# Kernel tuning notes

Measured on AMD Instinct MI355X. Metric: run time of the kernel, lower is better.

Reference implementation:

```python
import jax, jax.numpy as jnp
import numpy as np

NUM_NODES = 2048
NUM_UNITS = 64
INPUT_DIM = 2
MAX_K = 2  # max_diffusion_step


def setup_inputs() -> dict:
    key = jax.random.key(0)
    ks = jax.random.split(key, 8)
    B, N, U, D = 32, NUM_NODES, NUM_UNITS, INPUT_DIM
    C = D + U                      # input_size after concat = 66
    M = 2 * MAX_K + 1              # num_matrices = 5
    w_scale = 1.0 / np.sqrt(C * M)
    return {
        "inputs": jax.random.normal(ks[0], (B, N * D), dtype=jnp.float32),
        "hx": jax.random.normal(ks[1], (B, N * U), dtype=jnp.float32),
        # row-stochastic-ish random-walk supports (scaled so K hops stay bounded)
        "support0": jax.random.uniform(ks[2], (N, N), dtype=jnp.float32) / N,
        "support1": jax.random.uniform(ks[3], (N, N), dtype=jnp.float32) / N,
        "W_ru": jax.random.normal(ks[4], (C * M, 2 * U), dtype=jnp.float32) * w_scale,
        "b_ru": jnp.full((2 * U,), 1.0, dtype=jnp.float32),   # bias_start=1.0
        "W_c": jax.random.normal(ks[5], (C * M, U), dtype=jnp.float32) * w_scale,
        "b_c": jnp.zeros((U,), dtype=jnp.float32),            # bias_start=0.0
    }


def _gconv(inputs, state, supports, W, b, output_size):
    # inputs: [B, N*D], state: [B, N*U]
    B = inputs.shape[0]
    N = NUM_NODES
    x0 = jnp.concatenate(
        [inputs.reshape(B, N, -1), state.reshape(B, N, -1)], axis=2
    )  # [B, N, C]
    C = x0.shape[2]
    xs = [x0]
    for S in supports:  # Chebyshev-style diffusion per support
        x1 = jnp.einsum("nm,bmc->bnc", S, x0)
        xs.append(x1)
        xk1, xk2 = x1, x0
        for _ in range(2, MAX_K + 1):
            x2 = 2.0 * jnp.einsum("nm,bmc->bnc", S, xk1) - xk2
            xs.append(x2)
            xk1, xk2 = x2, xk1
    M = len(xs)  # num_matrices
    # stack on new leading axis then permute(1,2,3,0): feature-major, matrix-minor
    x = jnp.stack(xs, axis=0).transpose(1, 2, 3, 0).reshape(B * N, C * M)
    out = x @ W + b  # [B*N, output_size]
    return out.reshape(B, N * output_size)


def reference(inputs, hx, support0, support1, W_ru, b_ru, W_c, b_c):
    B = inputs.shape[0]
    N, U = NUM_NODES, NUM_UNITS
    supports = (support0, support1)
    value = jax.nn.sigmoid(_gconv(inputs, hx, supports, W_ru, b_ru, 2 * U))
    value = value.reshape(B, N, 2 * U)
    r = value[..., :U].reshape(B, N * U)
    u = value[..., U:].reshape(B, N * U)
    c = jnp.tanh(_gconv(inputs, r * hx, supports, W_c, b_c, U))
    new_state = u * hx + (1.0 - u) * c
    return new_state
```

## Files before the change

kernel.cpp:

```cpp
#include <hip/hip_runtime.h>
#include <hip/hip_bf16.h>
#include <cstdint>
#include <cstddef>

typedef unsigned short u16;
typedef unsigned char u8;
using f32x4 = __attribute__((ext_vector_type(4))) float;
using s16x8 = __attribute__((ext_vector_type(8))) short;
using s64x2 = __attribute__((ext_vector_type(2))) long;

#define NN 2048
#define BB 32
#define CC 66
#define JREAL 2112
#define JR 2176
#define KF 352
#define SROWS 65536

__device__ __forceinline__ int kperm(int k6) {
  return 16 * ((k6 >> 3) & 3) + 8 * (k6 >> 5) + (k6 & 7);
}

__device__ __forceinline__ float bf2f(u16 u) {
  union { uint32_t i; float f; } v; v.i = ((uint32_t)u) << 16; return v.f;
}
__device__ __forceinline__ u16 f2bf(float f) {
  union { float f; uint32_t i; } v; v.f = f;
  uint32_t x = v.i;
  x += 0x7fffu + ((x >> 16) & 1u);
  return (u16)(x >> 16);
}
__device__ __forceinline__ u8 f2e4m3(float x) {
  union { float f; uint32_t i; } v; v.f = x;
  uint32_t s = (v.i >> 24) & 0x80u;
  float a = fabsf(x);
  if (a >= 464.0f) return (u8)(s | 0x7Eu);
  if (a < 0.015625f) {
    int q = (int)rintf(a * 512.0f);
    return (u8)(s | (uint32_t)q);
  }
  union { float f; uint32_t i; } u; u.f = a;
  uint32_t lsb = (u.i >> 20) & 1u;
  u.i += 0x0007FFFFu + lsb;
  int e = (int)(u.i >> 23) - 127;
  uint32_t m = (u.i >> 20) & 7u;
  return (u8)(s | ((uint32_t)(e + 7) << 3) | m);
}

__device__ __forceinline__ void async_cp16(const u8* g, u8* l) {
  __builtin_amdgcn_global_load_lds(
      (const __attribute__((address_space(1))) unsigned int*)g,
      (__attribute__((address_space(3))) unsigned int*)l, 16, 0, 0);
}
__device__ __forceinline__ void async_cp16u(const u16* g, u16* l) {
  __builtin_amdgcn_global_load_lds(
      (const __attribute__((address_space(1))) unsigned int*)g,
      (__attribute__((address_space(3))) unsigned int*)l, 16, 0, 0);
}

template <int EPI>
__global__ __launch_bounds__(512, 2) void gemm_f8(
    const u8* __restrict__ A0, const u8* __restrict__ A1,
    const u8* __restrict__ A2, const u8* __restrict__ A3,
    const u8* __restrict__ B0, const u8* __restrict__ B1,
    const u8* __restrict__ B2, const u8* __restrict__ B3,
    void* __restrict__ C0, void* __restrict__ C1,
    void* __restrict__ C2, void* __restrict__ C3,
    int K, int lda, int ldb, int ldout, int mlimit)
{
  __shared__ u8 lds[3 * 25600];

  const int gx = gridDim.x, gy = gridDim.y;
  const int nwg = gx * gy * gridDim.z;
  const int orig = blockIdx.x + gx * (blockIdx.y + gy * blockIdx.z);
  const int cpx = nwg >> 3;
  const int swz = (orig & 7) * cpx + (orig >> 3);
  const int mb = swz % gx;
  const int t1 = swz / gx;
  const int nb = t1 % gy;
  const int zb = t1 / gy;

  const u8* A = (zb == 0) ? A0 : (zb == 1) ? A1 : (zb == 2) ? A2 : A3;
  const u8* B = (zb == 0) ? B0 : (zb == 1) ? B1 : (zb == 2) ? B2 : B3;
  void* Cv    = (zb == 0) ? C0 : (zb == 1) ? C1 : (zb == 2) ? C2 : C3;

  const int tid = threadIdx.x;
  const int wid = tid >> 6;
  const int lane = tid & 63;
  const int m0 = mb * 128;
  const int n0 = nb * 256;
  const int wm = (wid >> 2) * 64;
  const int wn = (wid & 3) * 64;

  const bool xtra = (EPI == 5) && (mb < 4);
  const int xrow0 = 2048 + mb * 16;
  const bool xw = xtra && (wid == 0);
  const bool xm = xtra && (wid < 4);

  const int srow = wid * 16 + (lane >> 2);
  const int sk   = ((lane & 3) ^ ((lane >> 3) & 3)) * 16;
  const u8* gA = A + (size_t)(m0 + srow) * lda + sk;
  const u8* gB = B + (size_t)(n0 + srow) * ldb + sk;
  const u8* gAx = A + (size_t)(xrow0 + (lane >> 2)) * lda + sk;
  u8* ldsA  = &lds[wid * 1024];
  u8* ldsB0 = &lds[8192 + wid * 1024];
  u8* ldsB1 = &lds[16384 + wid * 1024];
  u8* ldsAx = &lds[24576];

  const int r16 = lane & 15;
  const int hi = lane >> 4;
  const int rq = (r16 >> 1) & 3;
  const int goff = (hi ^ rq) * 16;
  const int abase = (wm + r16) * 64 + goff;
  const int bbase = 8192 + (wn + r16) * 64 + goff;
  const int xbase = 24576 + r16 * 64 + goff;

  f32x4 acc[4][4] = {};
  f32x4 accx[4] = {};
  const int nt = K >> 6;

#define STAGE(T_, SO_) { const int k0_ = (T_) * 64;                          \
    async_cp16(gA + k0_, ldsA + (SO_));                                      \
    async_cp16(gB + k0_, ldsB0 + (SO_));                                     \
    async_cp16(gB + (size_t)128 * ldb + k0_, ldsB1 + (SO_));                 \
    if (xw) async_cp16(gAx + k0_, ldsAx + (SO_)); }

  STAGE(0, 0);
  STAGE(1, 25600);
  if (xw) { asm volatile("s_waitcnt vmcnt(4)" ::: "memory"); }
  else    { asm volatile("s_waitcnt vmcnt(3)" ::: "memory"); }
  __builtin_amdgcn_s_barrier();

  int scur = 0;
  for (int t = 0; t < nt; ++t) {
    const int soff = scur * 25600;
    const bool more = (t + 2) < nt;
    if (more) {
      int sst = scur + 2; if (sst >= 3) sst -= 3;
      STAGE(t + 2, sst * 25600);
    }
    s64x2 af[4], bfr[4], axf;
#pragma unroll
    for (int mi = 0; mi < 4; ++mi)
      af[mi] = *(const s64x2*)&lds[soff + abase + mi * 1024];
#pragma unroll
    for (int ni = 0; ni < 4; ++ni)
      bfr[ni] = *(const s64x2*)&lds[soff + bbase + ni * 1024];
    if (xm) axf = *(const s64x2*)&lds[soff + xbase];
    __builtin_amdgcn_s_setprio(1);
#pragma unroll
    for (int h = 0; h < 2; ++h)
#pragma unroll
      for (int mi = 0; mi < 4; ++mi)
#pragma unroll
        for (int ni = 0; ni < 4; ++ni)
          acc[mi][ni] = __builtin_amdgcn_mfma_f32_16x16x32_fp8_fp8(
              af[mi][h], bfr[ni][h], acc[mi][ni], 0, 0, 0);
    if (xm) {
#pragma unroll
      for (int h = 0; h < 2; ++h)
#pragma unroll
        for (int ni = 0; ni < 4; ++ni)
          accx[ni] = __builtin_amdgcn_mfma_f32_16x16x32_fp8_fp8(
              axf[h], bfr[ni][h], accx[ni], 0, 0, 0);
    }
    __builtin_amdgcn_s_setprio(0);
    if (more) {
      if (xw) { asm volatile("s_waitcnt vmcnt(4)" ::: "memory"); }
      else    { asm volatile("s_waitcnt vmcnt(3)" ::: "memory"); }
    } else {
      asm volatile("s_waitcnt vmcnt(0)" ::: "memory");
    }
    __builtin_amdgcn_s_barrier();
    scur = (scur + 1 == 3) ? 0 : scur + 1;
  }
#undef STAGE

  const int lr = (lane >> 4) * 4;
  const int lc = lane & 15;

  if (EPI == 5) {
    u16* tl = (u16*)lds;
    u16* xc = (u16*)Cv;
    if (xm) {
#pragma unroll
      for (int ni = 0; ni < 4; ++ni) {
        const int ng = n0 + wn + ni * 16 + lc;
#pragma unroll
        for (int r = 0; r < 4; ++r) {
          const int c = xrow0 + lr + r - 2046;
          xc[((size_t)31 * NN + ng) * KF + (size_t)(zb + 1) * CC + c] =
              f2bf(accx[ni][r] * 0.00390625f);
        }
      }
    }
#pragma unroll
    for (int half = 0; half < 2; ++half) {
      __syncthreads();
      if ((wn >> 7) == half) {
#pragma unroll
        for (int mi = 0; mi < 4; ++mi)
#pragma unroll
          for (int ni = 0; ni < 4; ++ni) {
            const int np = (wn & 127) + ni * 16 + lc;
#pragma unroll
            for (int r = 0; r < 4; ++r) {
              const int j = wm + mi * 16 + lr + r;
              tl[np * 130 + j] = f2bf(acc[mi][ni][r] * 0.00390625f);
            }
          }
      }
      __syncthreads();
      for (int p = 0; p < 32; ++p) {
        const int idx = p * 512 + tid;
        const int jj = idx & 127;
        const int np = idx >> 7;
        const int j = m0 + jj;
        if (j < JREAL) {
          const int b = j / CC;
          const int c = j - b * CC;
          const int ng = n0 + half * 128 + np;
          xc[((size_t)b * NN + ng) * KF + (size_t)(zb + 1) * CC + c] =
              tl[np * 130 + jj];
        }
      }
    }
  } else {
#pragma unroll
    for (int mi = 0; mi < 4; ++mi)
#pragma unroll
      for (int ni = 0; ni < 4; ++ni) {
        const int colg = n0 + wn + ni * 16 + lc;
#pragma unroll
        for (int r = 0; r < 4; ++r) {
          const int rowg = m0 + wm + mi * 16 + lr + r;
          if (rowg < mlimit) {
            if (EPI == 0) {
              ((u16*)Cv)[(size_t)rowg * ldout + colg] =
                  f2bf(acc[mi][ni][r] * 0.00390625f);
            } else {
              float v = acc[mi][ni][r] * 0.0078125f -
                        ((rowg == colg) ? 256.0f : 0.0f);
              const int cpk = (colg & ~63) + kperm(colg & 63);
              ((u8*)Cv)[(size_t)rowg * ldout + cpk] = f2e4m3(v);
            }
          }
        }
      }
  }
}

__global__ __launch_bounds__(512, 2) void gemm_f8T(
    const u8* __restrict__ A0, const u8* __restrict__ A1,
    const u8* __restrict__ B0, const u8* __restrict__ B1,
    u8* __restrict__ C0, u8* __restrict__ C1,
    int K, int lda, int ldb, int ldout)
{
  __shared__ u8 lds[3 * 16384];

  const int gx = gridDim.x, gy = gridDim.y;
  const int nwg = gx * gy * gridDim.z;
  const int orig = blockIdx.x + gx * (blockIdx.y + gy * blockIdx.z);
  const int cpx = nwg >> 3;
  const int swz = (orig & 7) * cpx + (orig >> 3);
  const int mb = swz % gx;
  const int t1 = swz / gx;
  const int nb = t1 % gy;
  const int zb = t1 / gy;

  const u8* A = zb ? A1 : A0;
  const u8* B = zb ? B1 : B0;
  u8* C = zb ? C1 : C0;

  const int tid = threadIdx.x;
  const int wid = tid >> 6;
  const int lane = tid & 63;
  const int m0 = mb * 128;
  const int n0 = nb * 128;
  const int wm = (wid >> 2) * 64;
  const int wn = (wid & 3) * 32;

  const int srow = wid * 16 + (lane >> 2);
  const int sk   = ((lane & 3) ^ ((lane >> 3) & 3)) * 16;
  const u8* gA = A + (size_t)(m0 + srow) * lda + sk;
  const u8* gB = B + (size_t)(n0 + srow) * ldb + sk;
  u8* ldsA = &lds[wid * 1024];
  u8* ldsB = &lds[8192 + wid * 1024];

  const int r16 = lane & 15;
  const int hi = lane >> 4;
  const int rq = (r16 >> 1) & 3;
  const int goff = (hi ^ rq) * 16;
  const int abase = (wm + r16) * 64 + goff;
  const int bbase = 8192 + (wn + r16) * 64 + goff;

  f32x4 acc[4][2] = {};
  const int nt = K >> 6;

#define STAGE(T_, SO_) { const int k0_ = (T_) * 64;                          \
    async_cp16(gA + k0_, ldsA + (SO_));                                      \
    async_cp16(gB + k0_, ldsB + (SO_)); }

  STAGE(0, 0);
  STAGE(1, 16384);
  asm volatile("s_waitcnt vmcnt(2)" ::: "memory");
  __builtin_amdgcn_s_barrier();

  int scur = 0;
  for (int t = 0; t < nt; ++t) {
    const int soff = scur * 16384;
    const bool more = (t + 2) < nt;
    if (more) {
      int sst = scur + 2; if (sst >= 3) sst -= 3;
      STAGE(t + 2, sst * 16384);
    }
    s64x2 af[4], bfr[2];
#pragma unroll
    for (int mi = 0; mi < 4; ++mi)
      af[mi] = *(const s64x2*)&lds[soff + abase + mi * 1024];
#pragma unroll
    for (int ni = 0; ni < 2; ++ni)
      bfr[ni] = *(const s64x2*)&lds[soff + bbase + ni * 1024];
    __builtin_amdgcn_s_setprio(1);
#pragma unroll
    for (int h = 0; h < 2; ++h)
#pragma unroll
      for (int mi = 0; mi < 4; ++mi)
#pragma unroll
        for (int ni = 0; ni < 2; ++ni)
          acc[mi][ni] = __builtin_amdgcn_mfma_f32_16x16x32_fp8_fp8(
              af[mi][h], bfr[ni][h], acc[mi][ni], 0, 0, 0);
    __builtin_amdgcn_s_setprio(0);
    if (more) { asm volatile("s_waitcnt vmcnt(2)" ::: "memory"); }
    else      { asm volatile("s_waitcnt vmcnt(0)" ::: "memory"); }
    __builtin_amdgcn_s_barrier();
    scur = (scur + 1 == 3) ? 0 : scur + 1;
  }
#undef STAGE

  const int lr = (lane >> 4) * 4;
  const int lc = lane & 15;
#pragma unroll
  for (int mi = 0; mi < 4; ++mi)
#pragma unroll
    for (int ni = 0; ni < 2; ++ni) {
      const int colg = n0 + wn + ni * 16 + lc;
      const int cpk = (colg & ~63) + kperm(colg & 63);
#pragma unroll
      for (int r = 0; r < 4; ++r) {
        const int rowg = m0 + wm + mi * 16 + lr + r;
        float v = acc[mi][ni][r] * 0.0078125f -
                  ((rowg == colg) ? 256.0f : 0.0f);
        C[(size_t)rowg * ldout + cpk] = f2e4m3(v);
      }
    }
}

template <int EPI>
__global__ __launch_bounds__(256) void gemm_dense(
    const u16* __restrict__ A, const u16* __restrict__ B, u16* __restrict__ C,
    const float* __restrict__ bias,
    int K, int lda, int ldb, int ldout, int nstore)
{
  __shared__ u16 At[128 * 32];
  __shared__ u16 Bt[128 * 32];
  const int nwg = gridDim.x;
  const int orig = blockIdx.x;
  const int cpx = nwg >> 3;
  const int swz = (orig & 7) * cpx + (orig >> 3);
  const int mb = swz;

  const int tid = threadIdx.x;
  const int wid = tid >> 6;
  const int lane = tid & 63;
  const int m0 = mb * 128;
  const int wm = (wid >> 1) * 64;
  const int wn = (wid & 1) * 64;
  const int rA = lane >> 2;
  const int kA = ((lane & 3) ^ ((lane >> 3) & 3)) * 8;

  f32x4 acc[4][4] = {};

  const int c0 = wid * 2, c1 = wid * 2 + 1;
  const u16* gA0 = A + (size_t)(m0 + c0 * 16 + rA) * lda + kA;
  const u16* gA1 = A + (size_t)(m0 + c1 * 16 + rA) * lda + kA;
  const u16* gB0 = B + (size_t)(c0 * 16 + rA) * ldb + kA;
  const u16* gB1 = B + (size_t)(c1 * 16 + rA) * ldb + kA;

  for (int k0 = 0; k0 < K; k0 += 32) {
    async_cp16u(gA0 + k0, &At[c0 * 512]);
    async_cp16u(gA1 + k0, &At[c1 * 512]);
    async_cp16u(gB0 + k0, &Bt[c0 * 512]);
    async_cp16u(gB1 + k0, &Bt[c1 * 512]);
    __syncthreads();
    s16x8 af[4], bfr[4];
    const int r16 = lane & 15;
    const int cswz = ((lane >> 4) ^ ((r16 >> 1) & 3)) << 3;
#pragma unroll
    for (int mi = 0; mi < 4; ++mi)
      af[mi] = *(const s16x8*)&At[(wm + mi * 16 + r16) * 32 + cswz];
#pragma unroll
    for (int ni = 0; ni < 4; ++ni)
      bfr[ni] = *(const s16x8*)&Bt[(wn + ni * 16 + r16) * 32 + cswz];
#pragma unroll
    for (int mi = 0; mi < 4; ++mi)
#pragma unroll
      for (int ni = 0; ni < 4; ++ni)
        acc[mi][ni] = __builtin_amdgcn_mfma_f32_16x16x32_bf16(af[mi], bfr[ni], acc[mi][ni], 0, 0, 0);
    __syncthreads();
  }

  const int lr = (lane >> 4) * 4;
  const int lc = lane & 15;
#pragma unroll
  for (int mi = 0; mi < 4; ++mi) {
#pragma unroll
    for (int ni = 0; ni < 4; ++ni) {
      const int colg = wn + ni * 16 + lc;
#pragma unroll
      for (int r = 0; r < 4; ++r) {
        const int rowg = m0 + wm + mi * 16 + lr + r;
        float v = acc[mi][ni][r];
        if (EPI == 2) { v += bias[colg]; v = 1.0f / (1.0f + __expf(-v)); }
        if (EPI == 3) { v += bias[colg]; v = tanhf(v); }
        if (colg < nstore)
          C[(size_t)rowg * ldout + colg] = f2bf(v);
      }
    }
  }
}

__global__ __launch_bounds__(256) void cvt_S(const float* __restrict__ Sa,
                                             const float* __restrict__ Sb,
                                             u8* __restrict__ Sha, u8* __restrict__ Shb,
                                             u8* __restrict__ Sta, u8* __restrict__ Stb) {
  __shared__ u8 tile[64 * 68];
  const float* S = blockIdx.z ? Sb : Sa;
  u8* Sh = blockIdx.z ? Shb : Sha;
  u8* St = blockIdx.z ? Stb : Sta;
  const int c0 = blockIdx.x * 64;
  const int r0 = blockIdx.y * 64;
  const int t = threadIdx.x;
#pragma unroll
  for (int p = 0; p < 4; ++p) {
    const int idx = p * 256 + t;
    const int r = idx >> 4;
    const int c4 = (idx & 15) * 4;
    float4 v = *reinterpret_cast<const float4*>(S + (size_t)(r0 + r) * NN + c0 + c4);
    union { u8 b[4]; uint32_t w; } o;
    o.b[0] = f2e4m3(v.x * 256.0f); o.b[1] = f2e4m3(v.y * 256.0f);
    o.b[2] = f2e4m3(v.z * 256.0f); o.b[3] = f2e4m3(v.w * 256.0f);
    *reinterpret_cast<uint32_t*>(Sh + (size_t)(r0 + r) * NN + c0 + kperm(c4)) = o.w;
    *reinterpret_cast<uint32_t*>(&tile[r * 68 + c4]) = o.w;
  }
  __syncthreads();
  const int cc = t >> 2;
#pragma unroll
  for (int half = 0; half < 2; ++half) {
    const int j = (t & 3) * 2 + half;
    union { u8 b[8]; uint64_t w; } buf;
#pragma unroll
    for (int i = 0; i < 8; ++i) buf.b[i] = tile[(j * 8 + i) * 68 + cc];
    const int npos = 16 * (j & 3) + 8 * (j >> 2);
    *reinterpret_cast<uint64_t*>(St + (size_t)(c0 + cc) * NN + r0 + npos) = buf.w;
  }
}

__global__ __launch_bounds__(256) void build_wt(const float* __restrict__ W,
                                                u16* __restrict__ Wt, int ocols) {
  int t = blockIdx.x * 256 + threadIdx.x;
  if (t >= 128 * KF) return;
  int o = t / KF, kf = t - o * KF;
  float v = 0.0f;
  if (kf < 330 && o < ocols) {
    int m = kf / CC, c = kf - m * CC;
    v = W[(size_t)(c * 5 + m) * ocols + o];
  }
  Wt[t] = f2bf(v);
}

__global__ __launch_bounds__(256) void pack_x0(const float* __restrict__ inputs,
                                               const float* __restrict__ hx,
                                               const u16* __restrict__ ru,
                                               u8* __restrict__ X0t,
                                               u16* __restrict__ xcat, int useR) {
  __shared__ u16 tile[128 * 76];
  const int n0 = blockIdx.x * 128;
  const int b = blockIdx.y;
  const int t = threadIdx.x;
#pragma unroll
  for (int p = 0; p < 8; ++p) {
    const int idx = p * 256 + t;
    const int n = idx >> 4;
    const int u4 = (idx & 15) * 4;
    float4 v = *reinterpret_cast<const float4*>(
        hx + (size_t)b * (NN * 64) + (size_t)(n0 + n) * 64 + u4);
    if (useR) {
      ushort4 rv = *reinterpret_cast<const ushort4*>(
          ru + ((size_t)b * NN + n0 + n) * 128 + u4);
      v.x *= bf2f(rv.x); v.y *= bf2f(rv.y); v.z *= bf2f(rv.z); v.w *= bf2f(rv.w);
    }
    ushort4 o;
    o.x = f2bf(v.x); o.y = f2bf(v.y); o.z = f2bf(v.z); o.w = f2bf(v.w);
    *reinterpret_cast<ushort4*>(&tile[n * 76 + u4]) = o;
  }
  __syncthreads();
#pragma unroll
  for (int p = 0; p < 33; ++p) {
    const int idx = p * 256 + t;
    const int c = idx >> 7;
    const int n = idx & 127;
    float val;
    if (c < 2) val = inputs[(size_t)b * (NN * 2) + (size_t)(n0 + n) * 2 + c];
    else       val = bf2f(tile[n * 76 + (c - 2)]);
    const int np = (n & ~63) + kperm(n & 63);
    X0t[(size_t)(b * CC + c) * NN + n0 + np] = f2e4m3(val);
  }
#pragma unroll
  for (int p = 0; p < 17; ++p) {
    const int idx = p * 256 + t;
    if (idx < 128 * 33) {
      const int n = idx / 33;
      const int pr = idx - n * 33;
      const int col = pr * 2;
      u16 v0, v1;
      if (col == 0) {
        v0 = f2bf(inputs[(size_t)b * (NN * 2) + (size_t)(n0 + n) * 2 + 0]);
        v1 = f2bf(inputs[(size_t)b * (NN * 2) + (size_t)(n0 + n) * 2 + 1]);
      } else {
        v0 = tile[n * 76 + (col - 2)];
        v1 = tile[n * 76 + (col - 1)];
      }
      ushort2 o2; o2.x = v0; o2.y = v1;
      *reinterpret_cast<ushort2*>(
          xcat + ((size_t)b * NN + n0 + n) * KF + col) = o2;
    }
  }
}

__global__ __launch_bounds__(256) void final_k(const float* __restrict__ hx,
                                               const u16* __restrict__ ru,
                                               const u16* __restrict__ cd,
                                               float* __restrict__ out) {
  size_t t = (size_t)blockIdx.x * 256 + threadIdx.x;
  int u = (int)(t & 63);
  size_t s = t >> 6;
  float ug = bf2f(ru[s * 128 + 64 + u]);
  float cv = bf2f(cd[s * 64 + u]);
  float h = hx[t];
  out[t] = ug * h + (1.0f - ug) * cv;
}

extern "C" void kernel_launch(void* const* d_in, const int* in_sizes, int n_in,
                              void* d_out, int out_size, void* d_ws, size_t ws_size,
                              hipStream_t stream) {
  const float* inputs = (const float*)d_in[0];
  const float* hx     = (const float*)d_in[1];
  const float* S0     = (const float*)d_in[2];
  const float* S1     = (const float*)d_in[3];
  const float* Wru    = (const float*)d_in[4];
  const float* bru    = (const float*)d_in[5];
  const float* Wc     = (const float*)d_in[6];
  const float* bc     = (const float*)d_in[7];
  float* out = (float*)d_out;

  u8* ws8 = (u8*)d_ws;
  u8* S0h = ws8;
  u8* S1h = S0h + (size_t)NN * NN;
  u8* X0t = S1h + (size_t)NN * NN;
  u16* xcat = (u16*)(X0t + (size_t)JR * NN);
  u16* Wtru = xcat + (size_t)SROWS * KF;
  u16* Wtc  = Wtru + (size_t)128 * KF;
  u16* ru   = Wtc + (size_t)128 * KF;
  u16* cd   = ru + (size_t)SROWS * 128;
  u8* S0t = (u8*)xcat;
  u8* S1t = S0t + (size_t)NN * NN;
  u8* T0 = (u8*)d_out;
  u8* T1 = T0 + (size_t)NN * NN;

  dim3 b256(256);
  dim3 b512(512);
  cvt_S<<<dim3(NN / 64, NN / 64, 2), b256, 0, stream>>>(S0, S1, S0h, S1h, S0t, S1t);
  build_wt<<<dim3((128 * KF + 255) / 256), b256, 0, stream>>>(Wru, Wtru, 128);
  build_wt<<<dim3((128 * KF + 255) / 256), b256, 0, stream>>>(Wc, Wtc, 64);

  gemm_f8T<<<dim3(NN / 128, NN / 128, 2), b512, 0, stream>>>(
      S0h, S1h, S0t, S1t, T0, T1, NN, NN, NN, NN);

  const dim3 gdiff(16, NN / 256, 4);
  const dim3 gdense(SROWS / 128);
  const dim3 gpx0(NN / 128, BB);

  pack_x0<<<gpx0, b256, 0, stream>>>(inputs, hx, (const u16*)nullptr, X0t, xcat, 0);
  gemm_f8<5><<<gdiff, b512, 0, stream>>>(
      X0t, X0t, X0t, X0t,  S0h, T0, S1h, T1,
      (void*)xcat, (void*)xcat, (void*)xcat, (void*)xcat,
      NN, NN, NN, KF, JREAL);
  gemm_dense<2><<<gdense, b256, 0, stream>>>(xcat, Wtru, ru, bru, KF, KF, KF, 128, 128);

  pack_x0<<<gpx0, b256, 0, stream>>>(inputs, hx, ru, X0t, xcat, 1);
  gemm_f8<5><<<gdiff, b512, 0, stream>>>(
      X0t, X0t, X0t, X0t,  S0h, T0, S1h, T1,
      (void*)xcat, (void*)xcat, (void*)xcat, (void*)xcat,
      NN, NN, NN, KF, JREAL);
  gemm_dense<3><<<gdense, b256, 0, stream>>>(xcat, Wtc, cd, bc, KF, KF, KF, 64, 64);

  final_k<<<dim3(SROWS * 64 / 256), b256, 0, stream>>>(hx, ru, cd, out);
}
```

Measured before the change: 252.4 us.

## Split GEMM main loop into four barrier-separated phases interleaving loads and MFMAs

Restructures the fp8 MFMA main loop into four phases, one per B column block. Each phase issues one LDS fragment read and one async global-to-LDS copy for the next stage, then runs that block's MFMAs between workgroup barriers. The aim is to spread memory traffic across the compute and keep fewer B fragments in registers at once. In exchange it adds about seven extra barriers and lgkmcnt waits per iteration, which may serialize the waves and reduce MFMA throughput.

```diff
diff --git a/kernel.cpp b/kernel.cpp
--- a/kernel.cpp
+++ b/kernel.cpp
@@ -119,14 +119,14 @@
   f32x4 accx[4] = {};
   const int nt = K >> 6;
 
-#define STAGE(T_, SO_) { const int k0_ = (T_) * 64;                          \
+#define STAGE_ALL(T_, SO_) { const int k0_ = (T_) * 64;                      \
     async_cp16(gA + k0_, ldsA + (SO_));                                      \
     async_cp16(gB + k0_, ldsB0 + (SO_));                                     \
     async_cp16(gB + (size_t)128 * ldb + k0_, ldsB1 + (SO_));                 \
     if (xw) async_cp16(gAx + k0_, ldsAx + (SO_)); }
 
-  STAGE(0, 0);
-  STAGE(1, 25600);
+  STAGE_ALL(0, 0);
+  STAGE_ALL(1, 25600);
   if (xw) { asm volatile("s_waitcnt vmcnt(4)" ::: "memory"); }
   else    { asm volatile("s_waitcnt vmcnt(3)" ::: "memory"); }
   __builtin_amdgcn_s_barrier();
@@ -135,34 +135,80 @@
   for (int t = 0; t < nt; ++t) {
     const int soff = scur * 25600;
     const bool more = (t + 2) < nt;
-    if (more) {
-      int sst = scur + 2; if (sst >= 3) sst -= 3;
-      STAGE(t + 2, sst * 25600);
-    }
-    s64x2 af[4], bfr[4], axf;
+    int sst = scur + 2; if (sst >= 3) sst -= 3;
+    const int so2 = sst * 25600;
+    const int k2 = (t + 2) * 64;
+
+    s64x2 af[4], bq, axf;
+
 #pragma unroll
     for (int mi = 0; mi < 4; ++mi)
       af[mi] = *(const s64x2*)&lds[soff + abase + mi * 1024];
-#pragma unroll
-    for (int ni = 0; ni < 4; ++ni)
-      bfr[ni] = *(const s64x2*)&lds[soff + bbase + ni * 1024];
+    bq = *(const s64x2*)&lds[soff + bbase];
     if (xm) axf = *(const s64x2*)&lds[soff + xbase];
+    if (more) async_cp16(gA + k2, ldsA + so2);
+    __builtin_amdgcn_s_barrier();
+    asm volatile("s_waitcnt lgkmcnt(0)" ::: "memory");
     __builtin_amdgcn_s_setprio(1);
 #pragma unroll
-    for (int h = 0; h < 2; ++h)
+    for (int h = 0; h < 2; ++h) {
 #pragma unroll
       for (int mi = 0; mi < 4; ++mi)
-#pragma unroll
-        for (int ni = 0; ni < 4; ++ni)
-          acc[mi][ni] = __builtin_amdgcn_mfma_f32_16x16x32_fp8_fp8(
-              af[mi][h], bfr[ni][h], acc[mi][ni], 0, 0, 0);
-    if (xm) {
-#pragma unroll
-      for (int h = 0; h < 2; ++h)
-#pragma unroll
-        for (int ni = 0; ni < 4; ++ni)
-          accx[ni] = __builtin_amdgcn_mfma_f32_16x16x32_fp8_fp8(
-              axf[h], bfr[ni][h], accx[ni], 0, 0, 0);
+        acc[mi][0] = __builtin_amdgcn_mfma_f32_16x16x32_fp8_fp8(
+            af[mi][h], bq[h], acc[mi][0], 0, 0, 0);
+      if (xm) accx[0] = __builtin_amdgcn_mfma_f32_16x16x32_fp8_fp8(
+            axf[h], bq[h], accx[0], 0, 0, 0);
+    }
+    __builtin_amdgcn_s_setprio(0);
+    __builtin_amdgcn_s_barrier();
+
+    bq = *(const s64x2*)&lds[soff + bbase + 1024];
+    if (more) async_cp16(gB + k2, ldsB0 + so2);
+    __builtin_amdgcn_s_barrier();
+    asm volatile("s_waitcnt lgkmcnt(0)" ::: "memory");
+    __builtin_amdgcn_s_setprio(1);
+#pragma unroll
+    for (int h = 0; h < 2; ++h) {
+#pragma unroll
+      for (int mi = 0; mi < 4; ++mi)
+        acc[mi][1] = __builtin_amdgcn_mfma_f32_16x16x32_fp8_fp8(
+            af[mi][h], bq[h], acc[mi][1], 0, 0, 0);
+      if (xm) accx[1] = __builtin_amdgcn_mfma_f32_16x16x32_fp8_fp8(
+            axf[h], bq[h], accx[1], 0, 0, 0);
+    }
+    __builtin_amdgcn_s_setprio(0);
+    __builtin_amdgcn_s_barrier();
+
+    bq = *(const s64x2*)&lds[soff + bbase + 2048];
+    if (more) async_cp16(gB + (size_t)128 * ldb + k2, ldsB1 + so2);
+    __builtin_amdgcn_s_barrier();
+    asm volatile("s_waitcnt lgkmcnt(0)" ::: "memory");
+    __builtin_amdgcn_s_setprio(1);
+#pragma unroll
+    for (int h = 0; h < 2; ++h) {
+#pragma unroll
+      for (int mi = 0; mi < 4; ++mi)
+        acc[mi][2] = __builtin_amdgcn_mfma_f32_16x16x32_fp8_fp8(
+            af[mi][h], bq[h], acc[mi][2], 0, 0, 0);
+      if (xm) accx[2] = __builtin_amdgcn_mfma_f32_16x16x32_fp8_fp8(
+            axf[h], bq[h], accx[2], 0, 0, 0);
+    }
+    __builtin_amdgcn_s_setprio(0);
+    __builtin_amdgcn_s_barrier();
+
+    bq = *(const s64x2*)&lds[soff + bbase + 3072];
+    if (more && xw) async_cp16(gAx + k2, ldsAx + so2);
+    __builtin_amdgcn_s_barrier();
+    asm volatile("s_waitcnt lgkmcnt(0)" ::: "memory");
+    __builtin_amdgcn_s_setprio(1);
+#pragma unroll
+    for (int h = 0; h < 2; ++h) {
+#pragma unroll
+      for (int mi = 0; mi < 4; ++mi)
+        acc[mi][3] = __builtin_amdgcn_mfma_f32_16x16x32_fp8_fp8(
+            af[mi][h], bq[h], acc[mi][3], 0, 0, 0);
+      if (xm) accx[3] = __builtin_amdgcn_mfma_f32_16x16x32_fp8_fp8(
+            axf[h], bq[h], accx[3], 0, 0, 0);
     }
     __builtin_amdgcn_s_setprio(0);
     if (more) {
@@ -174,7 +220,7 @@
     __builtin_amdgcn_s_barrier();
     scur = (scur + 1 == 3) ? 0 : scur + 1;
   }
-#undef STAGE
+#undef STAGE_ALL
 
   const int lr = (lane >> 4) * 4;
   const int lc = lane & 15;
```

After: 237.8 us. -5.8%, faster.
